# Kernel optimization log

Hardware: AMD Instinct MI355X
Metric: run time of the kernel (lower is better)

Reference implementation:

```python
import jax, jax.numpy as jnp
import numpy as np
import math

EMBED_DIM = 768
NUM_HEADS = 12
HEAD_DIM = EMBED_DIM // NUM_HEADS
R = 16
LORA_ALPHA = 16
SCALING = LORA_ALPHA / math.sqrt(R)  # 4.0
U = 1.0  # ramp_up_steps=0 -> u()=1.0


def lora_linear(x, W, b, A):
    # base F.linear + SingLoRA delta: delta_W = A @ A.T (symmetric)
    base = x @ W.T + b
    delta_W = A @ A.T  # [D, D]
    return base + (x @ delta_W.T) * (U * SCALING)


def setup_inputs() -> dict:
    key = jax.random.key(0)
    ks = jax.random.split(key, 16)
    B, S, D = 2, 2048, EMBED_DIM
    inv = 1.0 / math.sqrt(D)
    d = {
        'query': jax.random.normal(ks[0], (B, S, D), jnp.float32),
        'key': jax.random.normal(ks[1], (B, S, D), jnp.float32),
        'value': jax.random.normal(ks[2], (B, S, D), jnp.float32),
        'Wq': jax.random.normal(ks[3], (D, D), jnp.float32) * inv,
        'bq': jax.random.normal(ks[4], (D,), jnp.float32) * 0.01,
        'Aq': jax.random.normal(ks[5], (D, R), jnp.float32) * 0.01,
        'Wk': jax.random.normal(ks[6], (D, D), jnp.float32) * inv,
        'bk': jax.random.normal(ks[7], (D,), jnp.float32) * 0.01,
        'Ak': jax.random.normal(ks[8], (D, R), jnp.float32) * 0.01,
        'Wv': jax.random.normal(ks[9], (D, D), jnp.float32) * inv,
        'bv': jax.random.normal(ks[10], (D,), jnp.float32) * 0.01,
        'Av': jax.random.normal(ks[11], (D, R), jnp.float32) * 0.01,
        'Wo': jax.random.normal(ks[12], (D, D), jnp.float32) * inv,
        'bo': jax.random.normal(ks[13], (D,), jnp.float32) * 0.01,
    }
    return d


def reference(query, key, value, Wq, bq, Aq, Wk, bk, Ak, Wv, bv, Av, Wo, bo):
    B, S, D = query.shape
    H, hd = NUM_HEADS, HEAD_DIM
    q = lora_linear(query, Wq, bq, Aq)
    k = lora_linear(key, Wk, bk, Ak)
    v = lora_linear(value, Wv, bv, Av)
    # [B, S, D] -> [B, H, S, hd]
    q = q.reshape(B, S, H, hd).transpose(0, 2, 1, 3)
    k = k.reshape(B, S, H, hd).transpose(0, 2, 1, 3)
    v = v.reshape(B, S, H, hd).transpose(0, 2, 1, 3)
    scores = jnp.einsum('bhqd,bhkd->bhqk', q, k) / math.sqrt(hd)
    attn = jax.nn.softmax(scores, axis=-1)
    out = jnp.einsum('bhqk,bhkd->bhqd', attn, v)  # [B, H, S, hd]
    out = out.transpose(0, 2, 1, 3).reshape(B, S, D)
    out = out @ Wo.T + bo
    return out
```

## Files before the change

kernel.cpp:

```cpp
#include <hip/hip_runtime.h>
#include <math.h>
#include <stdint.h>

#define D 768
#define S 2048
#define B_ 2
#define NROWS 4096
#define H 12
#define HD 64
#define R_ 16

typedef _Float16 half_t;
typedef _Float16 half8 __attribute__((ext_vector_type(8)));
typedef _Float16 half4 __attribute__((ext_vector_type(4)));
typedef float floatx4 __attribute__((ext_vector_type(4)));

#define MFMA32(a, b, c) __builtin_amdgcn_mfma_f32_16x16x32_f16(a, b, c, 0, 0, 0)
#define MFMA16(a, b, c) __builtin_amdgcn_mfma_f32_16x16x16f16(a, b, c, 0, 0, 0)

__device__ __forceinline__ void gl_lds16(const half_t* gp, half_t* lp) {
  __builtin_amdgcn_global_load_lds(
      (__attribute__((address_space(1))) void*)(gp),
      (__attribute__((address_space(3))) void*)(lp), 16, 0, 0);
}

__global__ __launch_bounds__(256) void prep_kernel(
    const float* __restrict__ q, const float* __restrict__ k,
    const float* __restrict__ v, half_t* __restrict__ xq,
    half_t* __restrict__ xk, half_t* __restrict__ xv,
    const float* __restrict__ Wq, const float* __restrict__ Aq,
    const float* __restrict__ Wk, const float* __restrict__ Ak,
    const float* __restrict__ Wv, const float* __restrict__ Av,
    const float* __restrict__ Wo, half_t* __restrict__ Mq,
    half_t* __restrict__ Mk, half_t* __restrict__ Mv,
    half_t* __restrict__ Mo) {
  const int bid = blockIdx.x;
  if (bid < 9216) {
    const int y = bid / 3072;
    const float* x = (y == 0) ? q : (y == 1) ? k : v;
    half_t* o = (y == 0) ? xq : (y == 1) ? xk : xv;
    int i = (bid - y * 3072) * 1024 + threadIdx.x * 4;
    float4 vv = *reinterpret_cast<const float4*>(x + i);
    half_t tmp[4] = {(half_t)vv.x, (half_t)vv.y, (half_t)vv.z, (half_t)vv.w};
    *reinterpret_cast<uint64_t*>(o + i) = *reinterpret_cast<uint64_t*>(tmp);
  } else {
    const int u = bid - 9216;
    const int y = u / 2304;
    const float* W = (y == 0) ? Wq : (y == 1) ? Wk : (y == 2) ? Wv : Wo;
    const float* A = (y == 0) ? Aq : (y == 1) ? Ak : (y == 2) ? Av : nullptr;
    half_t* M = (y == 0) ? Mq : (y == 1) ? Mk : (y == 2) ? Mv : Mo;
    int idx = (u - y * 2304) * 256 + threadIdx.x;
    int j = idx / D;
    int kk = idx - j * D;
    float acc = W[idx];
    if (A != nullptr) {
      float s = 0.f;
#pragma unroll
      for (int r = 0; r < R_; ++r) s += A[kk * R_ + r] * A[j * R_ + r];
      acc += 4.0f * s;
    }
    M[idx] = (half_t)acc;
  }
}

template <int RT, bool F32OUT, bool VT_Z2>
__global__ __launch_bounds__(256) void gemm_mfma_kernel(
    const half_t* __restrict__ x0, const half_t* __restrict__ x1,
    const half_t* __restrict__ x2, const half_t* __restrict__ m0,
    const half_t* __restrict__ m1, const half_t* __restrict__ m2,
    const float* __restrict__ b0, const float* __restrict__ b1,
    const float* __restrict__ b2, void* o0, void* o1, void* o2) {
  constexpr int RTILES = RT / 16;
  constexpr int AG = RTILES * 2;
  constexpr int G = AG + 16;
  constexpr int GPW = G / 4;
  constexpr int WC = (RT == 128) ? 2 : 4;
  constexpr int TPW = 4;
  constexpr int UPW = 8 / WC;
  constexpr int PB = G * 512;
  constexpr int TRS = 136;
  __shared__ __align__(16) half_t smem[2 * PB];

  const int z = blockIdx.z;
  const half_t* X = (z == 0) ? x0 : (z == 1) ? x1 : x2;
  const half_t* M = (z == 0) ? m0 : (z == 1) ? m1 : m2;
  const float* bias = (z == 0) ? b0 : (z == 1) ? b1 : b2;
  void* Out = (z == 0) ? o0 : (z == 1) ? o1 : o2;

  const int tid = threadIdx.x;
  const int lane = tid & 63;
  const int wv = tid >> 6;
  const int lr = lane & 15;
  const int lq = lane >> 4;
  const int row0 = blockIdx.y * RT;
  const int j0 = blockIdx.x * 128;
  const int wr = wv / WC;
  const int wc = wv % WC;

  floatx4 acc[TPW][UPW] = {};

#define GSTAGE(bufi, k0)                                                       \
  do {                                                                         \
    _Pragma("unroll") for (int gi = 0; gi < GPW; ++gi) {                       \
      int g = wv * GPW + gi;                                                   \
      if (g < AG) {                                                            \
        int t = g >> 1, c = g & 1;                                             \
        gl_lds16(                                                              \
            X + (size_t)(row0 + t * 16 + lr) * D + (k0) + c * 32 + lq * 8,     \
            smem + (bufi)*PB + g * 512);                                       \
      } else {                                                                 \
        int g2 = g - AG;                                                       \
        int u = g2 >> 1, c = g2 & 1;                                           \
        gl_lds16(                                                              \
            M + (size_t)(j0 + u * 16 + lr) * D + (k0) + c * 32 + lq * 8,       \
            smem + (bufi)*PB + AG * 512 + g2 * 512);                           \
      }                                                                        \
    }                                                                          \
  } while (0)

  GSTAGE(0, 0);
  __syncthreads();

  for (int it = 0; it < D / 64; ++it) {
    const int cur = it & 1;
    if (it + 1 < D / 64) GSTAGE(cur ^ 1, (it + 1) * 64);
    const half_t* Ab = smem + cur * PB;
    const half_t* Bb = Ab + AG * 512;
#pragma unroll
    for (int c = 0; c < 2; ++c) {
      half8 af[TPW], bf[UPW];
#pragma unroll
      for (int t = 0; t < TPW; ++t)
        af[t] = *reinterpret_cast<const half8*>(
            &Ab[(((wr * TPW + t) * 2 + c) * 64 + lane) * 8]);
#pragma unroll
      for (int u = 0; u < UPW; ++u)
        bf[u] = *reinterpret_cast<const half8*>(
            &Bb[(((wc * UPW + u) * 2 + c) * 64 + lane) * 8]);
#pragma unroll
      for (int t = 0; t < TPW; ++t)
#pragma unroll
        for (int u = 0; u < UPW; ++u) acc[t][u] = MFMA32(af[t], bf[u], acc[t][u]);
    }
    __syncthreads();
  }
#undef GSTAGE

  float bv[UPW];
#pragma unroll
  for (int u = 0; u < UPW; ++u) bv[u] = bias[j0 + (wc * UPW + u) * 16 + lr];

  if constexpr (VT_Z2 && RT == 128) {
    if (z == 2) {
#pragma unroll
      for (int t = 0; t < TPW; ++t) {
#pragma unroll
        for (int u = 0; u < UPW; ++u) {
          int c_local = (wc * UPW + u) * 16 + lr;
#pragma unroll
          for (int r = 0; r < 4; ++r) {
            int r_local = (wr * TPW + t) * 16 + lq * 4 + r;
            smem[c_local * TRS + r_local] = (half_t)(acc[t][u][r] + bv[u]);
          }
        }
      }
      __syncthreads();
      half_t* vt = (half_t*)Out;
      const int bb = row0 >> 11;
      const int s_base = row0 & 2047;
#pragma unroll
      for (int it = 0; it < 8; ++it) {
        int unit = it * 256 + tid;
        int c_local = unit >> 4;
        int chunk = unit & 15;
        half8 vv = *reinterpret_cast<const half8*>(
            &smem[c_local * TRS + chunk * 8]);
        int gc = j0 + c_local;
        int hh = gc >> 6, dd = gc & 63;
        *reinterpret_cast<half8*>(
            &vt[((size_t)(bb * H + hh) * HD + dd) * S + s_base + chunk * 8]) =
            vv;
      }
      return;
    }
  }

#pragma unroll
  for (int t = 0; t < TPW; ++t) {
#pragma unroll
    for (int u = 0; u < UPW; ++u) {
#pragma unroll
      for (int r = 0; r < 4; ++r) {
        int gr = row0 + (wr * TPW + t) * 16 + lq * 4 + r;
        int gc = j0 + (wc * UPW + u) * 16 + lr;
        float v = acc[t][u][r] + bv[u];
        if (F32OUT)
          ((float*)Out)[(size_t)gr * D + gc] = v;
        else
          ((half_t*)Out)[(size_t)gr * D + gc] = (half_t)v;
      }
    }
  }
}

__global__ __launch_bounds__(256) void attn_mfma_kernel(
    const half_t* __restrict__ Qh, const half_t* __restrict__ Kh,
    const half_t* __restrict__ Vt_g, half_t* __restrict__ Oh) {
  __shared__ __align__(16) half_t Ks[2][8 * 512];
  __shared__ __align__(16) half_t Vs[2][8 * 512];

  const int tid = threadIdx.x;
  const int lane = tid & 63;
  const int wv = tid >> 6;
  const int lr = lane & 15;
  const int lq = lane >> 4;
  const int q0 = blockIdx.x * 64;
  const int h = blockIdx.y;
  const int b = blockIdx.z;
  const size_t base = (size_t)b * S * D + h * HD;
  const size_t vtbase = (size_t)(b * H + h) * HD * (size_t)S;
  const int qw = q0 + wv * 16;

  half8 qf[2];
#pragma unroll
  for (int c = 0; c < 2; ++c) {
    half8 qv = *reinterpret_cast<const half8*>(
        &Qh[base + (size_t)(qw + lr) * D + c * 32 + lq * 8]);
#pragma unroll
    for (int j = 0; j < 8; ++j) qv[j] = qv[j] * (half_t)0.125f;
    qf[c] = qv;
  }

  floatx4 o[4] = {};
  float lsum = 0.f;

#define STAGE(bufi, kb)                                                        \
  do {                                                                         \
    _Pragma("unroll") for (int gi = 0; gi < 2; ++gi) {                         \
      int g = wv * 2 + gi;                                                     \
      int u = g >> 1, c = g & 1;                                               \
      gl_lds16(Kh + base + (size_t)((kb) + u * 16 + lr) * D + c * 32 + lq * 8, \
               &Ks[bufi][g * 512]);                                            \
      gl_lds16(                                                                \
          Vt_g + vtbase + (size_t)(u * 16 + lr) * S + (kb) + c * 32 + lq * 8,  \
          &Vs[bufi][g * 512]);                                                 \
    }                                                                          \
  } while (0)

  STAGE(0, 0);
  __syncthreads();

  for (int it = 0; it < S / 64; ++it) {
    const int cur = it & 1;
    if (it + 1 < S / 64) STAGE(cur ^ 1, (it + 1) * 64);

#pragma unroll
    for (int u = 0; u < 4; ++u) {
      half8 kf0 = *reinterpret_cast<const half8*>(
          &Ks[cur][((u * 2 + 0) * 64 + lane) * 8]);
      half8 kf1 = *reinterpret_cast<const half8*>(
          &Ks[cur][((u * 2 + 1) * 64 + lane) * 8]);
      floatx4 st = {};
      st = MFMA32(kf0, qf[0], st);
      st = MFMA32(kf1, qf[1], st);
      float p0 = __expf(st[0]);
      float p1 = __expf(st[1]);
      float p2 = __expf(st[2]);
      float p3 = __expf(st[3]);
      lsum += (p0 + p1) + (p2 + p3);
      half4 pf;
      pf[0] = (half_t)p0; pf[1] = (half_t)p1;
      pf[2] = (half_t)p2; pf[3] = (half_t)p3;
#pragma unroll
      for (int ud = 0; ud < 4; ++ud) {
        half4 vf = *reinterpret_cast<const half4*>(
            &Vs[cur][(ud * 2 + (u >> 1)) * 512 +
                     ((((u & 1) * 2) + (lq >> 1)) * 16 + lr) * 8 +
                     (lq & 1) * 4]);
        o[ud] = MFMA16(pf, vf, o[ud]);
      }
    }
    __syncthreads();
  }
#undef STAGE

  lsum += __shfl_xor(lsum, 16);
  lsum += __shfl_xor(lsum, 32);

  float linv[4];
#pragma unroll
  for (int r = 0; r < 4; ++r) linv[r] = 1.0f / __shfl(lsum, lq * 4 + r);
#pragma unroll
  for (int ud = 0; ud < 4; ++ud) {
#pragma unroll
    for (int r = 0; r < 4; ++r) {
      int row = qw + lq * 4 + r;
      int col = h * HD + ud * 16 + lr;
      Oh[(size_t)(b * S + row) * D + col] = (half_t)(o[ud][r] * linv[r]);
    }
  }
}

extern "C" void kernel_launch(void* const* d_in, const int* in_sizes, int n_in,
                              void* d_out, int out_size, void* d_ws,
                              size_t ws_size, hipStream_t stream) {
  const float* query = (const float*)d_in[0];
  const float* key   = (const float*)d_in[1];
  const float* value = (const float*)d_in[2];
  const float* Wq = (const float*)d_in[3];
  const float* bq = (const float*)d_in[4];
  const float* Aq = (const float*)d_in[5];
  const float* Wk = (const float*)d_in[6];
  const float* bk = (const float*)d_in[7];
  const float* Ak = (const float*)d_in[8];
  const float* Wv = (const float*)d_in[9];
  const float* bv = (const float*)d_in[10];
  const float* Av = (const float*)d_in[11];
  const float* Wo = (const float*)d_in[12];
  const float* bo = (const float*)d_in[13];
  float* out = (float*)d_out;

  half_t* hw = (half_t*)d_ws;
  const size_t XSZ = (size_t)NROWS * D;
  const size_t MSZ = (size_t)D * D;
  half_t* xq = hw;
  half_t* xk = xq + XSZ;
  half_t* xv = xk + XSZ;
  half_t* qh = xv + XSZ;
  half_t* kh = qh + XSZ;
  half_t* vt = kh + XSZ;
  half_t* ab = vt + XSZ;
  half_t* Mq = ab + XSZ;
  half_t* Mk = Mq + MSZ;
  half_t* Mv = Mk + MSZ;
  half_t* Mo = Mv + MSZ;

  prep_kernel<<<18432, 256, 0, stream>>>(query, key, value, xq, xk, xv, Wq, Aq,
                                         Wk, Ak, Wv, Av, Wo, Mq, Mk, Mv, Mo);

  dim3 gq(D / 128, NROWS / 128, 3);
  gemm_mfma_kernel<128, false, true><<<gq, 256, 0, stream>>>(
      xq, xk, xv, Mq, Mk, Mv, bq, bk, bv, qh, kh, vt);

  dim3 ga(S / 64, H, B_);
  attn_mfma_kernel<<<ga, 256, 0, stream>>>(qh, kh, vt, ab);

  dim3 go(D / 128, NROWS / 64, 1);
  gemm_mfma_kernel<64, true, false><<<go, 256, 0, stream>>>(
      ab, ab, ab, Mo, Mo, Mo, bo, bo, bo, out, out, out);
}
```

Before: 233.6 us.

## Fuse fp32-to-fp16 input conversion into QKV GEMM and split attention KV across waves

The separate pass that converted the query, key and value activations to fp16 is removed. The QKV GEMM now loads fp32 activations through registers, converts them, and writes them to LDS, which saves one full write and read of the activations. The attention kernel grows to 512 threads, with two wave halves each handling half of every KV tile and their results combined through LDS. It also switches to exp2 with a prescaled Q, and computes the row sums with an MFMA against a ones vector. Risks include register pressure from the staged fp32 A loads and added reduction and synchronisation overhead.

```diff
diff --git a/kernel.cpp b/kernel.cpp
--- a/kernel.cpp
+++ b/kernel.cpp
@@ -17,96 +17,220 @@
 
 #define MFMA32(a, b, c) __builtin_amdgcn_mfma_f32_16x16x32_f16(a, b, c, 0, 0, 0)
 #define MFMA16(a, b, c) __builtin_amdgcn_mfma_f32_16x16x16f16(a, b, c, 0, 0, 0)
-
-__device__ __forceinline__ void gl_lds16(const half_t* gp, half_t* lp) {
+#define EXP2F(x) __builtin_amdgcn_exp2f(x)
+
+__device__ __forceinline__ void gl_lds16(const void* gp, half_t* lp) {
   __builtin_amdgcn_global_load_lds(
-      (__attribute__((address_space(1))) void*)(gp),
+      (const __attribute__((address_space(1))) void*)(gp),
       (__attribute__((address_space(3))) void*)(lp), 16, 0, 0);
 }
 
-__global__ __launch_bounds__(256) void prep_kernel(
-    const float* __restrict__ q, const float* __restrict__ k,
-    const float* __restrict__ v, half_t* __restrict__ xq,
-    half_t* __restrict__ xk, half_t* __restrict__ xv,
+__global__ __launch_bounds__(256) void build_M4_kernel(
     const float* __restrict__ Wq, const float* __restrict__ Aq,
     const float* __restrict__ Wk, const float* __restrict__ Ak,
     const float* __restrict__ Wv, const float* __restrict__ Av,
     const float* __restrict__ Wo, half_t* __restrict__ Mq,
     half_t* __restrict__ Mk, half_t* __restrict__ Mv,
     half_t* __restrict__ Mo) {
-  const int bid = blockIdx.x;
-  if (bid < 9216) {
-    const int y = bid / 3072;
-    const float* x = (y == 0) ? q : (y == 1) ? k : v;
-    half_t* o = (y == 0) ? xq : (y == 1) ? xk : xv;
-    int i = (bid - y * 3072) * 1024 + threadIdx.x * 4;
-    float4 vv = *reinterpret_cast<const float4*>(x + i);
-    half_t tmp[4] = {(half_t)vv.x, (half_t)vv.y, (half_t)vv.z, (half_t)vv.w};
-    *reinterpret_cast<uint64_t*>(o + i) = *reinterpret_cast<uint64_t*>(tmp);
-  } else {
-    const int u = bid - 9216;
-    const int y = u / 2304;
-    const float* W = (y == 0) ? Wq : (y == 1) ? Wk : (y == 2) ? Wv : Wo;
-    const float* A = (y == 0) ? Aq : (y == 1) ? Ak : (y == 2) ? Av : nullptr;
-    half_t* M = (y == 0) ? Mq : (y == 1) ? Mk : (y == 2) ? Mv : Mo;
-    int idx = (u - y * 2304) * 256 + threadIdx.x;
-    int j = idx / D;
-    int kk = idx - j * D;
-    float acc = W[idx];
-    if (A != nullptr) {
-      float s = 0.f;
-#pragma unroll
-      for (int r = 0; r < R_; ++r) s += A[kk * R_ + r] * A[j * R_ + r];
-      acc += 4.0f * s;
-    }
-    M[idx] = (half_t)acc;
-  }
-}
-
-template <int RT, bool F32OUT, bool VT_Z2>
-__global__ __launch_bounds__(256) void gemm_mfma_kernel(
-    const half_t* __restrict__ x0, const half_t* __restrict__ x1,
-    const half_t* __restrict__ x2, const half_t* __restrict__ m0,
+  const int y = blockIdx.y;
+  const float* W = (y == 0) ? Wq : (y == 1) ? Wk : (y == 2) ? Wv : Wo;
+  const float* A = (y == 0) ? Aq : (y == 1) ? Ak : (y == 2) ? Av : nullptr;
+  half_t* M = (y == 0) ? Mq : (y == 1) ? Mk : (y == 2) ? Mv : Mo;
+  int idx = blockIdx.x * 256 + threadIdx.x;
+  int j = idx / D;
+  int kk = idx - j * D;
+  float acc = W[idx];
+  if (A != nullptr) {
+    float s = 0.f;
+#pragma unroll
+    for (int r = 0; r < R_; ++r) s += A[kk * R_ + r] * A[j * R_ + r];
+    acc += 4.0f * s;
+  }
+  M[idx] = (half_t)acc;
+}
+
+__global__ __launch_bounds__(256) void gemm_qkv_kernel(
+    const float* __restrict__ x0, const float* __restrict__ x1,
+    const float* __restrict__ x2, const half_t* __restrict__ m0,
     const half_t* __restrict__ m1, const half_t* __restrict__ m2,
     const float* __restrict__ b0, const float* __restrict__ b1,
-    const float* __restrict__ b2, void* o0, void* o1, void* o2) {
-  constexpr int RTILES = RT / 16;
-  constexpr int AG = RTILES * 2;
-  constexpr int G = AG + 16;
-  constexpr int GPW = G / 4;
-  constexpr int WC = (RT == 128) ? 2 : 4;
-  constexpr int TPW = 4;
-  constexpr int UPW = 8 / WC;
-  constexpr int PB = G * 512;
+    const float* __restrict__ b2, half_t* __restrict__ o0,
+    half_t* __restrict__ o1, half_t* __restrict__ o2) {
+  constexpr int PB = 32 * 512;
   constexpr int TRS = 136;
   __shared__ __align__(16) half_t smem[2 * PB];
 
   const int z = blockIdx.z;
-  const half_t* X = (z == 0) ? x0 : (z == 1) ? x1 : x2;
+  const float* X = (z == 0) ? x0 : (z == 1) ? x1 : x2;
   const half_t* M = (z == 0) ? m0 : (z == 1) ? m1 : m2;
   const float* bias = (z == 0) ? b0 : (z == 1) ? b1 : b2;
-  void* Out = (z == 0) ? o0 : (z == 1) ? o1 : o2;
+  half_t* Out = (z == 0) ? o0 : (z == 1) ? o1 : o2;
 
   const int tid = threadIdx.x;
   const int lane = tid & 63;
   const int wv = tid >> 6;
   const int lr = lane & 15;
   const int lq = lane >> 4;
-  const int row0 = blockIdx.y * RT;
+  const int row0 = blockIdx.y * 128;
   const int j0 = blockIdx.x * 128;
-  const int wr = wv / WC;
-  const int wc = wv % WC;
-
-  floatx4 acc[TPW][UPW] = {};
+  const int wr = wv >> 1;
+  const int wc = wv & 1;
+
+  const int g_ = tid >> 4;
+  const int a_ = tid & 15;
+  const int arow0 = row0 + (g_ >> 1) * 16 + (a_ & 3) * 4;
+  const int acolb = (g_ & 1) * 32 + (a_ >> 2) * 8;
+
+  floatx4 acc[4][4] = {};
+  float4 ra[8];
+
+#define LOADA(k0)                                                              \
+  do {                                                                         \
+    _Pragma("unroll") for (int i = 0; i < 4; ++i) {                            \
+      const float* p = X + (size_t)(arow0 + i) * D + (k0) + acolb;             \
+      ra[2 * i] = *reinterpret_cast<const float4*>(p);                         \
+      ra[2 * i + 1] = *reinterpret_cast<const float4*>(p + 4);                 \
+    }                                                                          \
+  } while (0)
+
+#define WRITEA(bufi)                                                           \
+  do {                                                                         \
+    _Pragma("unroll") for (int i = 0; i < 4; ++i) {                            \
+      half8 hh;                                                                \
+      hh[0] = (half_t)ra[2 * i].x;                                             \
+      hh[1] = (half_t)ra[2 * i].y;                                             \
+      hh[2] = (half_t)ra[2 * i].z;                                             \
+      hh[3] = (half_t)ra[2 * i].w;                                             \
+      hh[4] = (half_t)ra[2 * i + 1].x;                                         \
+      hh[5] = (half_t)ra[2 * i + 1].y;                                         \
+      hh[6] = (half_t)ra[2 * i + 1].z;                                         \
+      hh[7] = (half_t)ra[2 * i + 1].w;                                         \
+      *reinterpret_cast<half8*>(smem + (bufi)*PB + 32 * tid + 8 * i) = hh;     \
+    }                                                                          \
+  } while (0)
+
+#define STAGEB(bufi, k0)                                                       \
+  do {                                                                         \
+    _Pragma("unroll") for (int gi = 0; gi < 4; ++gi) {                         \
+      int gb = wv * 4 + gi;                                                    \
+      int u = gb >> 1, cb = gb & 1;                                            \
+      gl_lds16(M + (size_t)(j0 + u * 16 + lr) * D + (k0) + cb * 32 + lq * 8,   \
+               smem + (bufi)*PB + 16 * 512 + gb * 512);                        \
+    }                                                                          \
+  } while (0)
+
+  STAGEB(0, 0);
+  LOADA(0);
+  WRITEA(0);
+  __syncthreads();
+
+  for (int it = 0; it < D / 64; ++it) {
+    const int cur = it & 1;
+    if (it + 1 < D / 64) {
+      STAGEB(cur ^ 1, (it + 1) * 64);
+      LOADA((it + 1) * 64);
+    }
+    const half_t* Ab = smem + cur * PB;
+    const half_t* Bb = Ab + 16 * 512;
+#pragma unroll
+    for (int c = 0; c < 2; ++c) {
+      half8 af[4], bf[4];
+#pragma unroll
+      for (int t = 0; t < 4; ++t)
+        af[t] = *reinterpret_cast<const half8*>(
+            &Ab[(((wr * 4 + t) * 2 + c) * 64 + lane) * 8]);
+#pragma unroll
+      for (int u = 0; u < 4; ++u)
+        bf[u] = *reinterpret_cast<const half8*>(
+            &Bb[(((wc * 4 + u) * 2 + c) * 64 + lane) * 8]);
+#pragma unroll
+      for (int t = 0; t < 4; ++t)
+#pragma unroll
+        for (int u = 0; u < 4; ++u) acc[t][u] = MFMA32(af[t], bf[u], acc[t][u]);
+    }
+    if (it + 1 < D / 64) WRITEA(cur ^ 1);
+    __syncthreads();
+  }
+#undef LOADA
+#undef WRITEA
+#undef STAGEB
+
+  float bv[4];
+#pragma unroll
+  for (int u = 0; u < 4; ++u) bv[u] = bias[j0 + (wc * 4 + u) * 16 + lr];
+
+  if (z == 2) {
+#pragma unroll
+    for (int t = 0; t < 4; ++t) {
+#pragma unroll
+      for (int u = 0; u < 4; ++u) {
+        int c_local = (wc * 4 + u) * 16 + lr;
+#pragma unroll
+        for (int r = 0; r < 4; ++r) {
+          int r_local = (wr * 4 + t) * 16 + lq * 4 + r;
+          smem[c_local * TRS + r_local] = (half_t)(acc[t][u][r] + bv[u]);
+        }
+      }
+    }
+    __syncthreads();
+    const int bb = row0 >> 11;
+    const int s_base = row0 & 2047;
+#pragma unroll
+    for (int it = 0; it < 8; ++it) {
+      int unit = it * 256 + tid;
+      int c_local = unit >> 4;
+      int chunk = unit & 15;
+      half8 vv =
+          *reinterpret_cast<const half8*>(&smem[c_local * TRS + chunk * 8]);
+      int gc = j0 + c_local;
+      int hh = gc >> 6, dd = gc & 63;
+      *reinterpret_cast<half8*>(
+          &Out[((size_t)(bb * H + hh) * HD + dd) * S + s_base + chunk * 8]) = vv;
+    }
+    return;
+  }
+
+#pragma unroll
+  for (int t = 0; t < 4; ++t) {
+#pragma unroll
+    for (int u = 0; u < 4; ++u) {
+#pragma unroll
+      for (int r = 0; r < 4; ++r) {
+        int gr = row0 + (wr * 4 + t) * 16 + lq * 4 + r;
+        int gc = j0 + (wc * 4 + u) * 16 + lr;
+        Out[(size_t)gr * D + gc] = (half_t)(acc[t][u][r] + bv[u]);
+      }
+    }
+  }
+}
+
+__global__ __launch_bounds__(256) void gemm_o_kernel(
+    const half_t* __restrict__ Xh, const half_t* __restrict__ M,
+    const float* __restrict__ bias, float* __restrict__ Out) {
+  constexpr int AG = 8;
+  constexpr int G = AG + 16;
+  constexpr int PB = G * 512;
+  __shared__ __align__(16) half_t smem[2 * PB];
+
+  const int tid = threadIdx.x;
+  const int lane = tid & 63;
+  const int wv = tid >> 6;
+  const int lr = lane & 15;
+  const int lq = lane >> 4;
+  const int row0 = blockIdx.y * 64;
+  const int j0 = blockIdx.x * 128;
+  const int wc = wv;
+
+  floatx4 acc[4][2] = {};
 
 #define GSTAGE(bufi, k0)                                                       \
   do {                                                                         \
-    _Pragma("unroll") for (int gi = 0; gi < GPW; ++gi) {                       \
-      int g = wv * GPW + gi;                                                   \
+    _Pragma("unroll") for (int gi = 0; gi < 6; ++gi) {                         \
+      int g = wv * 6 + gi;                                                     \
       if (g < AG) {                                                            \
         int t = g >> 1, c = g & 1;                                             \
         gl_lds16(                                                              \
-            X + (size_t)(row0 + t * 16 + lr) * D + (k0) + c * 32 + lq * 8,     \
+            Xh + (size_t)(row0 + t * 16 + lr) * D + (k0) + c * 32 + lq * 8,    \
             smem + (bufi)*PB + g * 512);                                       \
       } else {                                                                 \
         int g2 = g - AG;                                                       \
@@ -128,90 +252,53 @@
     const half_t* Bb = Ab + AG * 512;
 #pragma unroll
     for (int c = 0; c < 2; ++c) {
-      half8 af[TPW], bf[UPW];
-#pragma unroll
-      for (int t = 0; t < TPW; ++t)
+      half8 af[4], bf[2];
+#pragma unroll
+      for (int t = 0; t < 4; ++t)
         af[t] = *reinterpret_cast<const half8*>(
-            &Ab[(((wr * TPW + t) * 2 + c) * 64 + lane) * 8]);
-#pragma unroll
-      for (int u = 0; u < UPW; ++u)
+            &Ab[((t * 2 + c) * 64 + lane) * 8]);
+#pragma unroll
+      for (int u = 0; u < 2; ++u)
         bf[u] = *reinterpret_cast<const half8*>(
-            &Bb[(((wc * UPW + u) * 2 + c) * 64 + lane) * 8]);
-#pragma unroll
-      for (int t = 0; t < TPW; ++t)
-#pragma unroll
-        for (int u = 0; u < UPW; ++u) acc[t][u] = MFMA32(af[t], bf[u], acc[t][u]);
+            &Bb[(((wc * 2 + u) * 2 + c) * 64 + lane) * 8]);
+#pragma unroll
+      for (int t = 0; t < 4; ++t)
+#pragma unroll
+        for (int u = 0; u < 2; ++u) acc[t][u] = MFMA32(af[t], bf[u], acc[t][u]);
     }
     __syncthreads();
   }
 #undef GSTAGE
 
-  float bv[UPW];
-#pragma unroll
-  for (int u = 0; u < UPW; ++u) bv[u] = bias[j0 + (wc * UPW + u) * 16 + lr];
-
-  if constexpr (VT_Z2 && RT == 128) {
-    if (z == 2) {
-#pragma unroll
-      for (int t = 0; t < TPW; ++t) {
-#pragma unroll
-        for (int u = 0; u < UPW; ++u) {
-          int c_local = (wc * UPW + u) * 16 + lr;
-#pragma unroll
-          for (int r = 0; r < 4; ++r) {
-            int r_local = (wr * TPW + t) * 16 + lq * 4 + r;
-            smem[c_local * TRS + r_local] = (half_t)(acc[t][u][r] + bv[u]);
-          }
-        }
+  float bv[2];
+#pragma unroll
+  for (int u = 0; u < 2; ++u) bv[u] = bias[j0 + (wc * 2 + u) * 16 + lr];
+#pragma unroll
+  for (int t = 0; t < 4; ++t) {
+#pragma unroll
+    for (int u = 0; u < 2; ++u) {
+#pragma unroll
+      for (int r = 0; r < 4; ++r) {
+        int gr = row0 + t * 16 + lq * 4 + r;
+        int gc = j0 + (wc * 2 + u) * 16 + lr;
+        Out[(size_t)gr * D + gc] = acc[t][u][r] + bv[u];
       }
-      __syncthreads();
-      half_t* vt = (half_t*)Out;
-      const int bb = row0 >> 11;
-      const int s_base = row0 & 2047;
-#pragma unroll
-      for (int it = 0; it < 8; ++it) {
-        int unit = it * 256 + tid;
-        int c_local = unit >> 4;
-        int chunk = unit & 15;
-        half8 vv = *reinterpret_cast<const half8*>(
-            &smem[c_local * TRS + chunk * 8]);
-        int gc = j0 + c_local;
-        int hh = gc >> 6, dd = gc & 63;
-        *reinterpret_cast<half8*>(
-            &vt[((size_t)(bb * H + hh) * HD + dd) * S + s_base + chunk * 8]) =
-            vv;
-      }
-      return;
-    }
-  }
-
-#pragma unroll
-  for (int t = 0; t < TPW; ++t) {
-#pragma unroll
-    for (int u = 0; u < UPW; ++u) {
-#pragma unroll
-      for (int r = 0; r < 4; ++r) {
-        int gr = row0 + (wr * TPW + t) * 16 + lq * 4 + r;
-        int gc = j0 + (wc * UPW + u) * 16 + lr;
-        float v = acc[t][u][r] + bv[u];
-        if (F32OUT)
-          ((float*)Out)[(size_t)gr * D + gc] = v;
-        else
-          ((half_t*)Out)[(size_t)gr * D + gc] = (half_t)v;
-      }
-    }
-  }
-}
-
-__global__ __launch_bounds__(256) void attn_mfma_kernel(
+    }
+  }
+}
+
+__global__ __launch_bounds__(512, 6) void attn_mfma_kernel(
     const half_t* __restrict__ Qh, const half_t* __restrict__ Kh,
     const half_t* __restrict__ Vt_g, half_t* __restrict__ Oh) {
-  __shared__ __align__(16) half_t Ks[2][8 * 512];
-  __shared__ __align__(16) half_t Vs[2][8 * 512];
+  __shared__ __align__(16) half_t smem[16384];
+  half_t* Ks = smem;
+  half_t* Vs = smem + 8192;
 
   const int tid = threadIdx.x;
   const int lane = tid & 63;
   const int wv = tid >> 6;
+  const int t_ = wv & 3;
+  const int half_ = wv >> 2;
   const int lr = lane & 15;
   const int lq = lane >> 4;
   const int q0 = blockIdx.x * 64;
@@ -219,31 +306,43 @@
   const int b = blockIdx.z;
   const size_t base = (size_t)b * S * D + h * HD;
   const size_t vtbase = (size_t)(b * H + h) * HD * (size_t)S;
-  const int qw = q0 + wv * 16;
-
+  const int qw = q0 + t_ * 16;
+
+  const half_t qscale = (half_t)0.18033688f;
   half8 qf[2];
 #pragma unroll
   for (int c = 0; c < 2; ++c) {
     half8 qv = *reinterpret_cast<const half8*>(
         &Qh[base + (size_t)(qw + lr) * D + c * 32 + lq * 8]);
 #pragma unroll
-    for (int j = 0; j < 8; ++j) qv[j] = qv[j] * (half_t)0.125f;
+    for (int j = 0; j < 8; ++j) qv[j] = qv[j] * qscale;
     qf[c] = qv;
   }
 
+  half4 ones;
+#pragma unroll
+  for (int j = 0; j < 4; ++j) ones[j] = (half_t)1.0f;
+
   floatx4 o[4] = {};
-  float lsum = 0.f;
+  floatx4 ol = {};
 
 #define STAGE(bufi, kb)                                                        \
   do {                                                                         \
     _Pragma("unroll") for (int gi = 0; gi < 2; ++gi) {                         \
       int g = wv * 2 + gi;                                                     \
-      int u = g >> 1, c = g & 1;                                               \
-      gl_lds16(Kh + base + (size_t)((kb) + u * 16 + lr) * D + c * 32 + lq * 8, \
-               &Ks[bufi][g * 512]);                                            \
-      gl_lds16(                                                                \
-          Vt_g + vtbase + (size_t)(u * 16 + lr) * S + (kb) + c * 32 + lq * 8,  \
-          &Vs[bufi][g * 512]);                                                 \
+      if (g < 8) {                                                             \
+        int u = g >> 1, c = g & 1;                                             \
+        gl_lds16(                                                              \
+            Kh + base + (size_t)((kb) + u * 16 + lr) * D + c * 32 + lq * 8,    \
+            Ks + (bufi)*4096 + g * 512);                                       \
+      } else {                                                                 \
+        int gv = g - 8;                                                        \
+        int ud = gv >> 1, c = gv & 1;                                          \
+        gl_lds16(                                                              \
+            Vt_g + vtbase + (size_t)(ud * 16 + lr) * S + (kb) + c * 32 +       \
+                lq * 8,                                                        \
+            Vs + (bufi)*4096 + gv * 512);                                      \
+      }                                                                        \
     }                                                                          \
   } while (0)
 
@@ -255,48 +354,61 @@
     if (it + 1 < S / 64) STAGE(cur ^ 1, (it + 1) * 64);
 
 #pragma unroll
-    for (int u = 0; u < 4; ++u) {
+    for (int ui = 0; ui < 2; ++ui) {
+      const int u = half_ * 2 + ui;
       half8 kf0 = *reinterpret_cast<const half8*>(
-          &Ks[cur][((u * 2 + 0) * 64 + lane) * 8]);
+          &Ks[cur * 4096 + ((u * 2 + 0) * 64 + lane) * 8]);
       half8 kf1 = *reinterpret_cast<const half8*>(
-          &Ks[cur][((u * 2 + 1) * 64 + lane) * 8]);
+          &Ks[cur * 4096 + ((u * 2 + 1) * 64 + lane) * 8]);
       floatx4 st = {};
       st = MFMA32(kf0, qf[0], st);
       st = MFMA32(kf1, qf[1], st);
-      float p0 = __expf(st[0]);
-      float p1 = __expf(st[1]);
-      float p2 = __expf(st[2]);
-      float p3 = __expf(st[3]);
-      lsum += (p0 + p1) + (p2 + p3);
       half4 pf;
-      pf[0] = (half_t)p0; pf[1] = (half_t)p1;
-      pf[2] = (half_t)p2; pf[3] = (half_t)p3;
+      pf[0] = (half_t)EXP2F(st[0]);
+      pf[1] = (half_t)EXP2F(st[1]);
+      pf[2] = (half_t)EXP2F(st[2]);
+      pf[3] = (half_t)EXP2F(st[3]);
 #pragma unroll
       for (int ud = 0; ud < 4; ++ud) {
         half4 vf = *reinterpret_cast<const half4*>(
-            &Vs[cur][(ud * 2 + (u >> 1)) * 512 +
-                     ((((u & 1) * 2) + (lq >> 1)) * 16 + lr) * 8 +
-                     (lq & 1) * 4]);
+            &Vs[cur * 4096 + ((ud * 2 + (u >> 1)) * 64 +
+                              ((((u & 1) * 2) + (lq >> 1)) * 16 + lr)) *
+                                 8 +
+                (lq & 1) * 4]);
         o[ud] = MFMA16(pf, vf, o[ud]);
       }
+      ol = MFMA16(pf, ones, ol);
     }
     __syncthreads();
   }
 #undef STAGE
 
-  lsum += __shfl_xor(lsum, 16);
-  lsum += __shfl_xor(lsum, 32);
-
-  float linv[4];
-#pragma unroll
-  for (int r = 0; r < 4; ++r) linv[r] = 1.0f / __shfl(lsum, lq * 4 + r);
-#pragma unroll
-  for (int ud = 0; ud < 4; ++ud) {
-#pragma unroll
-    for (int r = 0; r < 4; ++r) {
-      int row = qw + lq * 4 + r;
-      int col = h * HD + ud * 16 + lr;
-      Oh[(size_t)(b * S + row) * D + col] = (half_t)(o[ud][r] * linv[r]);
+  float* red = (float*)smem;
+  const int slot = t_ * 64 + lane;
+  if (half_ == 1) {
+#pragma unroll
+    for (int comp = 0; comp < 16; ++comp)
+      red[comp * 260 + slot] = o[comp >> 2][comp & 3];
+#pragma unroll
+    for (int r = 0; r < 4; ++r) red[(16 + r) * 260 + slot] = ol[r];
+  }
+  __syncthreads();
+  if (half_ == 0) {
+#pragma unroll
+    for (int comp = 0; comp < 16; ++comp)
+      o[comp >> 2][comp & 3] += red[comp * 260 + slot];
+    float linv[4];
+#pragma unroll
+    for (int r = 0; r < 4; ++r)
+      linv[r] = 1.0f / (ol[r] + red[(16 + r) * 260 + slot]);
+#pragma unroll
+    for (int ud = 0; ud < 4; ++ud) {
+#pragma unroll
+      for (int r = 0; r < 4; ++r) {
+        int row = qw + lq * 4 + r;
+        int col = h * HD + ud * 16 + lr;
+        Oh[(size_t)(b * S + row) * D + col] = (half_t)(o[ud][r] * linv[r]);
+      }
     }
   }
 }
@@ -323,10 +435,7 @@
   half_t* hw = (half_t*)d_ws;
   const size_t XSZ = (size_t)NROWS * D;
   const size_t MSZ = (size_t)D * D;
-  half_t* xq = hw;
-  half_t* xk = xq + XSZ;
-  half_t* xv = xk + XSZ;
-  half_t* qh = xv + XSZ;
+  half_t* qh = hw;
   half_t* kh = qh + XSZ;
   half_t* vt = kh + XSZ;
   half_t* ab = vt + XSZ;
@@ -335,17 +444,17 @@
   half_t* Mv = Mk + MSZ;
   half_t* Mo = Mv + MSZ;
 
-  prep_kernel<<<18432, 256, 0, stream>>>(query, key, value, xq, xk, xv, Wq, Aq,
-                                         Wk, Ak, Wv, Av, Wo, Mq, Mk, Mv, Mo);
+  dim3 gm(D * D / 256, 4);
+  build_M4_kernel<<<gm, 256, 0, stream>>>(Wq, Aq, Wk, Ak, Wv, Av, Wo, Mq, Mk,
+                                          Mv, Mo);
 
   dim3 gq(D / 128, NROWS / 128, 3);
-  gemm_mfma_kernel<128, false, true><<<gq, 256, 0, stream>>>(
-      xq, xk, xv, Mq, Mk, Mv, bq, bk, bv, qh, kh, vt);
+  gemm_qkv_kernel<<<gq, 256, 0, stream>>>(query, key, value, Mq, Mk, Mv, bq,
+                                          bk, bv, qh, kh, vt);
 
   dim3 ga(S / 64, H, B_);
-  attn_mfma_kernel<<<ga, 256, 0, stream>>>(qh, kh, vt, ab);
+  attn_mfma_kernel<<<ga, 512, 0, stream>>>(qh, kh, vt, ab);
 
   dim3 go(D / 128, NROWS / 64, 1);
-  gemm_mfma_kernel<64, true, false><<<go, 256, 0, stream>>>(
-      ab, ab, ab, Mo, Mo, Mo, bo, bo, bo, out, out, out);
-}
+  gemm_o_kernel<<<go, 256, 0, stream>>>(ab, Mo, bo, out);
+}
```

After: 243.5 us. +4.2%, slower.
